# Kernel optimization log

Measured on AMD Instinct MI355X. Metric: run time of the kernel, lower is better.

## Reference

```python
import jax, jax.numpy as jnp
import numpy as np

B = 8192
W = 48            # target-net width
P = 4849          # flat param size of target MLP(1->48->48->48->1)
HW = 96           # hypernet width = 2*W
STEPS = 20
LR = 0.1
B1, B2, EPS = 0.9, 0.999, 1e-8


def setup_inputs() -> dict:
    key = jax.random.key(0)
    ks = jax.random.split(key, 6)
    x = jax.random.normal(ks[0], (B, 1), dtype=jnp.float32)
    c = jax.random.normal(ks[1], (B, 1), dtype=jnp.float32)
    # hypernet params (Linear(2,96) -> relu -> Linear(96,4849)), He-ish scaling
    hw1 = jax.random.normal(ks[2], (HW, 2), dtype=jnp.float32) / jnp.sqrt(2.0)
    hb1 = jax.random.normal(ks[3], (HW,), dtype=jnp.float32) * 0.1
    hw2 = jax.random.normal(ks[4], (P, HW), dtype=jnp.float32) / jnp.sqrt(float(HW))
    hb2 = jax.random.normal(ks[5], (P,), dtype=jnp.float32) * 0.1
    return {"x": x, "c": c, "hw1": hw1, "hb1": hb1, "hw2": hw2, "hb2": hb2}


def _target_apply(p, y):
    # unflatten per tree_flatten order: (w,b) per Linear layer of MLP(1,48,48,48,1)
    w0 = p[0:48].reshape(W, 1);      b0 = p[48:96]
    w1 = p[96:2400].reshape(W, W);   b1 = p[2400:2448]
    w2 = p[2448:4752].reshape(W, W); b2 = p[4752:4800]
    w3 = p[4800:4848].reshape(1, W); b3 = p[4848:4849]
    h = jax.nn.swish(w0 @ y + b0)
    h = jax.nn.swish(w1 @ h + b1)
    h = jax.nn.swish(w2 @ h + b2)
    return jnp.squeeze(w3 @ h + b3)


def _taylor_energy_y(energy_fn, y_target, y_anchor):
    # 2nd-order Taylor expansion via nested JVPs (order_y == 2)
    tangent = y_target - y_anchor

    def grad_energy(y):
        return jax.jvp(energy_fn, (y,), (tangent,))[1]

    e0, term1 = jax.jvp(energy_fn, (y_anchor,), (tangent,))
    _, term2 = jax.jvp(grad_energy, (y_anchor,), (tangent,))
    return e0 + term1 + 0.5 * term2


def _energy(y, p, y_anchor):
    return _taylor_energy_y(lambda yi: _target_apply(p, yi), y, y_anchor)


_grad_fn = jax.vmap(jax.grad(_energy), in_axes=(0, 0, 0))  # grad wrt y only


def reference(x, c, hw1, hb1, hw2, hb2):
    hyper_in = jnp.concatenate([x, c], axis=1)                 # (B, 2)
    h = jax.nn.relu(hyper_in @ hw1.T + hb1)                    # (B, 96)
    flat_params = h @ hw2.T + hb2                              # (B, P)

    y0 = jnp.zeros((x.shape[0], 1), dtype=x.dtype)             # y_mean = 0.0
    m0 = jnp.zeros_like(y0)
    v0 = jnp.zeros_like(y0)

    def step(carry, _):
        y, m, v, t = carry
        g = _grad_fn(y, flat_params, y)  # key=None -> anchor y0 = y_curr
        t = t + 1
        m = B1 * m + (1.0 - B1) * g
        v = B2 * v + (1.0 - B2) * g * g
        mh = m / (1.0 - jnp.power(B1, t))
        vh = v / (1.0 - jnp.power(B2, t))
        y = y - LR * mh / (jnp.sqrt(vh) + EPS)
        return (y, m, v, t), None

    (y_final, _, _, _), _ = jax.lax.scan(
        step, (y0, m0, v0, jnp.asarray(0, jnp.int32)), None, length=STEPS)
    return y_final
```

## Files before the change

kernel.cpp:

```cpp
#include <hip/hip_runtime.h>
#include <cstdint>
#include <cstddef>

#define NB    8192
#define NP    4849
#define NW    48
#define NCH   38
#define GY    16

typedef __attribute__((ext_vector_type(8))) _Float16 f16x8;
typedef __attribute__((ext_vector_type(4))) float f32x4;
typedef __attribute__((ext_vector_type(2))) float f32x2;

__device__ __forceinline__ const float* pptr(const float* Pp, int i, int rp) {
  return Pp + ((size_t)(rp >> 7) * NB + i) * 128 + (rp & 127);
}

__device__ __forceinline__ int invperm(int rp) {
  if (rp >= 96 && rp < 2400) {
    int t = rp - 96; int kb = t / 192; int rem = t - kb * 192;
    return 96 + (rem >> 2) * 48 + (kb * 4 + (rem & 3));
  }
  if (rp >= 2448 && rp < 4752) {
    int t = rp - 2448; int kb = t / 192; int rem = t - kb * 192;
    return 2448 + (rem >> 2) * 48 + (kb * 4 + (rem & 3));
  }
  return rp;
}

__global__ __launch_bounds__(256, 2) void hyper_gemm(
    const float* __restrict__ x, const float* __restrict__ c,
    const float* __restrict__ hw1, const float* __restrict__ hb1,
    const float* __restrict__ hw2, const float* __restrict__ hb2,
    float* __restrict__ Pp)
{
  const int t    = threadIdx.x;
  const int lane = t & 63;
  const int wv   = t >> 6;
  const int m16  = lane & 15;
  const int q    = lane >> 4;
  const int rp0  = blockIdx.x * 128;

  const float* wr[2];
  float bias[2];
  #pragma unroll
  for (int nt = 0; nt < 2; ++nt) {
    int rp = rp0 + wv * 32 + nt * 16 + m16;
    int r  = (rp < NP) ? invperm(rp) : 0;
    wr[nt]   = hw2 + (size_t)r * 96;
    bias[nt] = (rp < NP) ? hb2[r] : 0.f;
  }

  f16x8 bh[3][2], bl[3][2];
  #pragma unroll
  for (int ch = 0; ch < 3; ++ch) {
    const int k0 = ch * 32 + q * 8;
    #pragma unroll
    for (int nt = 0; nt < 2; ++nt) {
      float4 f0 = *(const float4*)(wr[nt] + k0);
      float4 f1 = *(const float4*)(wr[nt] + k0 + 4);
      float fv[8] = {f0.x,f0.y,f0.z,f0.w,f1.x,f1.y,f1.z,f1.w};
      #pragma unroll
      for (int e = 0; e < 8; ++e) {
        _Float16 hi = (_Float16)fv[e];
        float r = fv[e] - (float)hi;
        bh[ch][nt][e] = hi;
        bl[ch][nt][e] = (_Float16)r;
      }
    }
  }

  float* cbase = Pp + (size_t)blockIdx.x * NB * 128;

  for (int mtile = blockIdx.y; mtile < 128; mtile += GY) {
    const int i0 = mtile * 64;

    float xv[4], cv[4];
    #pragma unroll
    for (int mt = 0; mt < 4; ++mt) {
      int i = i0 + mt * 16 + m16;
      xv[mt] = x[i]; cv[mt] = c[i];
    }

    f32x4 acc[4][2];
    #pragma unroll
    for (int mt = 0; mt < 4; ++mt)
      #pragma unroll
      for (int nt = 0; nt < 2; ++nt)
        acc[mt][nt] = (f32x4){0.f, 0.f, 0.f, 0.f};

    #pragma unroll
    for (int ch = 0; ch < 3; ++ch) {
      const int k0 = ch * 32 + q * 8;

      float4 A0 = *(const float4*)(hw1 + 2 * k0);
      float4 A1 = *(const float4*)(hw1 + 2 * k0 + 4);
      float4 A2 = *(const float4*)(hw1 + 2 * k0 + 8);
      float4 A3 = *(const float4*)(hw1 + 2 * k0 + 12);
      float4 B0 = *(const float4*)(hb1 + k0);
      float4 B1 = *(const float4*)(hb1 + k0 + 4);
      float w0k[8] = {A0.x,A0.z,A1.x,A1.z,A2.x,A2.z,A3.x,A3.z};
      float w1k[8] = {A0.y,A0.w,A1.y,A1.w,A2.y,A2.w,A3.y,A3.w};
      float bk[8]  = {B0.x,B0.y,B0.z,B0.w,B1.x,B1.y,B1.z,B1.w};

      f16x8 ah[4], al[4];
      #pragma unroll
      for (int mt = 0; mt < 4; ++mt) {
        #pragma unroll
        for (int j = 0; j < 8; ++j) {
          float h = fmaf(xv[mt], w0k[j], fmaf(cv[mt], w1k[j], bk[j]));
          h = h > 0.f ? h : 0.f;
          _Float16 hi = (_Float16)h;
          float r = h - (float)hi;
          ah[mt][j] = hi;
          al[mt][j] = (_Float16)r;
        }
      }

      #pragma unroll
      for (int mt = 0; mt < 4; ++mt)
        #pragma unroll
        for (int nt = 0; nt < 2; ++nt) {
          acc[mt][nt] = __builtin_amdgcn_mfma_f32_16x16x32_f16(al[mt], bl[ch][nt], acc[mt][nt], 0, 0, 0);
          acc[mt][nt] = __builtin_amdgcn_mfma_f32_16x16x32_f16(ah[mt], bl[ch][nt], acc[mt][nt], 0, 0, 0);
          acc[mt][nt] = __builtin_amdgcn_mfma_f32_16x16x32_f16(al[mt], bh[ch][nt], acc[mt][nt], 0, 0, 0);
          acc[mt][nt] = __builtin_amdgcn_mfma_f32_16x16x32_f16(ah[mt], bh[ch][nt], acc[mt][nt], 0, 0, 0);
        }
    }

    #pragma unroll
    for (int nt = 0; nt < 2; ++nt) {
      int off = wv * 32 + nt * 16 + m16;
      if (rp0 + off < NP) {
        #pragma unroll
        for (int mt = 0; mt < 4; ++mt)
          #pragma unroll
          for (int r = 0; r < 4; ++r) {
            int i = i0 + mt * 16 + q * 4 + r;
            cbase[(size_t)i * 128 + off] = acc[mt][nt][r] + bias[nt];
          }
      }
    }
  }
}


#define DPP_ADD(x, ctrl, rmask)                                               \
  (x) += __int_as_float(__builtin_amdgcn_update_dpp(                          \
      0, __float_as_int(x), (ctrl), (rmask), 0xf, false))

#define RDLANE(x, k) __int_as_float(__builtin_amdgcn_readlane(__float_as_int(x), (k)))

__global__ __launch_bounds__(256, 2) void adam_inner(
    const float* __restrict__ Pp, float* __restrict__ out)
{
  const int lane = threadIdx.x & 63;
  const int wv   = threadIdx.x >> 6;
  const int i    = blockIdx.x * 4 + wv;
  const bool act = lane < NW;

  float w0  = act ? *pptr(Pp, i, lane)        : 0.f;
  float b0  = act ? *pptr(Pp, i, 48 + lane)   : 0.f;
  float b1v = act ? *pptr(Pp, i, 2400 + lane) : 0.f;
  float b2v = act ? *pptr(Pp, i, 4752 + lane) : 0.f;
  float w3  = act ? *pptr(Pp, i, 4800 + lane) : 0.f;

  f32x2 w1p[24], w2p[24];
  #pragma unroll
  for (int kb = 0; kb < 12; ++kb) {
    float4 q1 = *(const float4*)pptr(Pp, i, 96 + kb * 192 + lane * 4);
    w1p[2 * kb]     = (f32x2){q1.x, q1.y};
    w1p[2 * kb + 1] = (f32x2){q1.z, q1.w};
    float4 q2 = *(const float4*)pptr(Pp, i, 2448 + kb * 192 + lane * 4);
    w2p[2 * kb]     = (f32x2){q2.x, q2.y};
    w2p[2 * kb + 1] = (f32x2){q2.z, q2.w};
  }

  float y = 0.f, m = 0.f, v = 0.f;
  float b1t = 1.f, b2t = 1.f;

  #pragma unroll 1
  for (int t = 0; t < 20; ++t) {
    float z  = fmaf(w0, y, b0);
    float s  = __builtin_amdgcn_rcpf(1.f + __expf(-z));
    float h1 = z * s;
    float dh1 = fmaf(h1, 1.f - s, s) * w0;

    float za = b1v, zb = 0.f, da = 0.f, db = 0.f;
    #pragma unroll
    for (int k2 = 0; k2 < 24; ++k2) {
      float hk0 = RDLANE(h1,  2 * k2);
      float hk1 = RDLANE(h1,  2 * k2 + 1);
      float dk0 = RDLANE(dh1, 2 * k2);
      float dk1 = RDLANE(dh1, 2 * k2 + 1);
      za = fmaf(w1p[k2].x, hk0, za);
      zb = fmaf(w1p[k2].y, hk1, zb);
      da = fmaf(w1p[k2].x, dk0, da);
      db = fmaf(w1p[k2].y, dk1, db);
    }
    float z1  = za + zb;
    float dz1 = da + db;

    s = __builtin_amdgcn_rcpf(1.f + __expf(-z1));
    float h2  = z1 * s;
    float dh2 = fmaf(h2, 1.f - s, s) * dz1;

    za = b2v; zb = 0.f; da = 0.f; db = 0.f;
    #pragma unroll
    for (int k2 = 0; k2 < 24; ++k2) {
      float hk0 = RDLANE(h2,  2 * k2);
      float hk1 = RDLANE(h2,  2 * k2 + 1);
      float dk0 = RDLANE(dh2, 2 * k2);
      float dk1 = RDLANE(dh2, 2 * k2 + 1);
      za = fmaf(w2p[k2].x, hk0, za);
      zb = fmaf(w2p[k2].y, hk1, zb);
      da = fmaf(w2p[k2].x, dk0, da);
      db = fmaf(w2p[k2].y, dk1, db);
    }
    float z2  = za + zb;
    float dz2 = da + db;

    s = __builtin_amdgcn_rcpf(1.f + __expf(-z2));
    float dh3 = fmaf(z2 * s, 1.f - s, s) * dz2;

    float r = act ? w3 * dh3 : 0.f;
    DPP_ADD(r, 0x111, 0xf);
    DPP_ADD(r, 0x112, 0xf);
    DPP_ADD(r, 0x114, 0xf);
    DPP_ADD(r, 0x118, 0xf);
    DPP_ADD(r, 0x142, 0xa);
    DPP_ADD(r, 0x143, 0xc);
    float g = RDLANE(r, 63);

    m = fmaf(0.9f,   m, 0.1f   * g);
    v = fmaf(0.999f, v, 0.001f * g * g);
    b1t *= 0.9f; b2t *= 0.999f;
    float mh  = m * __builtin_amdgcn_rcpf(1.f - b1t);
    float vh  = v * __builtin_amdgcn_rcpf(1.f - b2t);
    float den = __builtin_amdgcn_sqrtf(vh) + 1e-8f;
    y -= 0.1f * mh * __builtin_amdgcn_rcpf(den);
  }

  if (lane == 0) out[i] = y;
}

extern "C" void kernel_launch(void* const* d_in, const int* in_sizes, int n_in,
                              void* d_out, int out_size, void* d_ws, size_t ws_size,
                              hipStream_t stream) {
  const float* x   = (const float*)d_in[0];
  const float* c   = (const float*)d_in[1];
  const float* hw1 = (const float*)d_in[2];
  const float* hb1 = (const float*)d_in[3];
  const float* hw2 = (const float*)d_in[4];
  const float* hb2 = (const float*)d_in[5];
  float* Pp  = (float*)d_ws;
  float* out = (float*)d_out;

  dim3 gridB(NCH, GY);
  hyper_gemm<<<gridB, dim3(256), 0, stream>>>(x, c, hw1, hb1, hw2, hb2, Pp);
  adam_inner<<<dim3(2048), dim3(256), 0, stream>>>(Pp, out);
}
```

Before: 237.3 us.

## Broadcast hidden activations through LDS and use one-wave blocks for inner loop

The inner Adam kernel now runs one 64-thread wave per sample block. The forward activations of each hidden layer are written to a small shared buffer and read back as float4 broadcasts, instead of being pulled out one lane at a time with readlane; the derivative path still uses readlane. The dot products now use four partial accumulators to shorten dependency chains, and the hyper GEMM grid gets more blocks along the batch dimension. The intent is to roughly halve the serial readlane traffic and raise parallelism, at the cost of LDS round trips and reliance on in-wave LDS ordering without a barrier.

```diff
diff --git a/kernel.cpp b/kernel.cpp
--- a/kernel.cpp
+++ b/kernel.cpp
@@ -6,7 +6,7 @@
 #define NP    4849
 #define NW    48
 #define NCH   38
-#define GY    16
+#define GY    64
 
 typedef __attribute__((ext_vector_type(8))) _Float16 f16x8;
 typedef __attribute__((ext_vector_type(4))) float f32x4;
@@ -151,12 +151,13 @@
 
 #define RDLANE(x, k) __int_as_float(__builtin_amdgcn_readlane(__float_as_int(x), (k)))
 
-__global__ __launch_bounds__(256, 2) void adam_inner(
+__global__ __launch_bounds__(64, 2) void adam_inner(
     const float* __restrict__ Pp, float* __restrict__ out)
 {
-  const int lane = threadIdx.x & 63;
-  const int wv   = threadIdx.x >> 6;
-  const int i    = blockIdx.x * 4 + wv;
+  __shared__ __align__(16) float hbuf[2][48];
+
+  const int lane = threadIdx.x;
+  const int i    = blockIdx.x;
   const bool act = lane < NW;
 
   float w0  = act ? *pptr(Pp, i, lane)        : 0.f;
@@ -181,44 +182,64 @@
 
   #pragma unroll 1
   for (int t = 0; t < 20; ++t) {
-    float z  = fmaf(w0, y, b0);
-    float s  = __builtin_amdgcn_rcpf(1.f + __expf(-z));
-    float h1 = z * s;
-    float dh1 = fmaf(h1, 1.f - s, s) * w0;
-
-    float za = b1v, zb = 0.f, da = 0.f, db = 0.f;
-    #pragma unroll
-    for (int k2 = 0; k2 < 24; ++k2) {
-      float hk0 = RDLANE(h1,  2 * k2);
-      float hk1 = RDLANE(h1,  2 * k2 + 1);
-      float dk0 = RDLANE(dh1, 2 * k2);
-      float dk1 = RDLANE(dh1, 2 * k2 + 1);
-      za = fmaf(w1p[k2].x, hk0, za);
-      zb = fmaf(w1p[k2].y, hk1, zb);
-      da = fmaf(w1p[k2].x, dk0, da);
-      db = fmaf(w1p[k2].y, dk1, db);
-    }
-    float z1  = za + zb;
-    float dz1 = da + db;
+    float z   = fmaf(w0, y, b0);
+    float s   = __builtin_amdgcn_rcpf(1.f + __expf(-z));
+    float h   = z * s;
+    float dh1 = fmaf(h, 1.f - s, s) * w0;
+    if (act) hbuf[0][lane] = h;
+
+    float z1, dz1;
+    {
+      float4 hq[12];
+      #pragma unroll
+      for (int kk = 0; kk < 12; ++kk)
+        hq[kk] = *(const float4*)(&hbuf[0][4 * kk]);
+      float zz[4] = {b1v, 0.f, 0.f, 0.f};
+      float dd[4] = {0.f, 0.f, 0.f, 0.f};
+      #pragma unroll
+      for (int kk = 0; kk < 12; ++kk) {
+        int c = kk & 3;
+        zz[c] = fmaf(w1p[2 * kk].x,     hq[kk].x, zz[c]);
+        zz[c] = fmaf(w1p[2 * kk].y,     hq[kk].y, zz[c]);
+        zz[c] = fmaf(w1p[2 * kk + 1].x, hq[kk].z, zz[c]);
+        zz[c] = fmaf(w1p[2 * kk + 1].y, hq[kk].w, zz[c]);
+        dd[c] = fmaf(w1p[2 * kk].x,     RDLANE(dh1, 4 * kk),     dd[c]);
+        dd[c] = fmaf(w1p[2 * kk].y,     RDLANE(dh1, 4 * kk + 1), dd[c]);
+        dd[c] = fmaf(w1p[2 * kk + 1].x, RDLANE(dh1, 4 * kk + 2), dd[c]);
+        dd[c] = fmaf(w1p[2 * kk + 1].y, RDLANE(dh1, 4 * kk + 3), dd[c]);
+      }
+      z1  = (zz[0] + zz[1]) + (zz[2] + zz[3]);
+      dz1 = (dd[0] + dd[1]) + (dd[2] + dd[3]);
+    }
 
     s = __builtin_amdgcn_rcpf(1.f + __expf(-z1));
     float h2  = z1 * s;
     float dh2 = fmaf(h2, 1.f - s, s) * dz1;
-
-    za = b2v; zb = 0.f; da = 0.f; db = 0.f;
-    #pragma unroll
-    for (int k2 = 0; k2 < 24; ++k2) {
-      float hk0 = RDLANE(h2,  2 * k2);
-      float hk1 = RDLANE(h2,  2 * k2 + 1);
-      float dk0 = RDLANE(dh2, 2 * k2);
-      float dk1 = RDLANE(dh2, 2 * k2 + 1);
-      za = fmaf(w2p[k2].x, hk0, za);
-      zb = fmaf(w2p[k2].y, hk1, zb);
-      da = fmaf(w2p[k2].x, dk0, da);
-      db = fmaf(w2p[k2].y, dk1, db);
-    }
-    float z2  = za + zb;
-    float dz2 = da + db;
+    if (act) hbuf[1][lane] = h2;
+
+    float z2, dz2;
+    {
+      float4 hq[12];
+      #pragma unroll
+      for (int kk = 0; kk < 12; ++kk)
+        hq[kk] = *(const float4*)(&hbuf[1][4 * kk]);
+      float zz[4] = {b2v, 0.f, 0.f, 0.f};
+      float dd[4] = {0.f, 0.f, 0.f, 0.f};
+      #pragma unroll
+      for (int kk = 0; kk < 12; ++kk) {
+        int c = kk & 3;
+        zz[c] = fmaf(w2p[2 * kk].x,     hq[kk].x, zz[c]);
+        zz[c] = fmaf(w2p[2 * kk].y,     hq[kk].y, zz[c]);
+        zz[c] = fmaf(w2p[2 * kk + 1].x, hq[kk].z, zz[c]);
+        zz[c] = fmaf(w2p[2 * kk + 1].y, hq[kk].w, zz[c]);
+        dd[c] = fmaf(w2p[2 * kk].x,     RDLANE(dh2, 4 * kk),     dd[c]);
+        dd[c] = fmaf(w2p[2 * kk].y,     RDLANE(dh2, 4 * kk + 1), dd[c]);
+        dd[c] = fmaf(w2p[2 * kk + 1].x, RDLANE(dh2, 4 * kk + 2), dd[c]);
+        dd[c] = fmaf(w2p[2 * kk + 1].y, RDLANE(dh2, 4 * kk + 3), dd[c]);
+      }
+      z2  = (zz[0] + zz[1]) + (zz[2] + zz[3]);
+      dz2 = (dd[0] + dd[1]) + (dd[2] + dd[3]);
+    }
 
     s = __builtin_amdgcn_rcpf(1.f + __expf(-z2));
     float dh3 = fmaf(z2 * s, 1.f - s, s) * dz2;
@@ -258,5 +279,5 @@
 
   dim3 gridB(NCH, GY);
   hyper_gemm<<<gridB, dim3(256), 0, stream>>>(x, c, hw1, hb1, hw2, hb2, Pp);
-  adam_inner<<<dim3(2048), dim3(256), 0, stream>>>(Pp, out);
-}
+  adam_inner<<<dim3(8192), dim3(64), 0, stream>>>(Pp, out);
+}
```

Result: faster. 220.0 us (-7.3%).
